# Optimization experiments

Measured on AMD Instinct MI355X. Metric: run time of the kernel, lower is better.

Reference implementation:

```python
import jax, jax.numpy as jnp
import numpy as np

OUT_DIM = 1024


def setup_inputs() -> dict:
    key = jax.random.key(0)
    k1, k2, k3, k4 = jax.random.split(key, 4)
    B, N, D = 4, 2048, 1024
    s = 1.0 / np.sqrt(D)
    return {
        "x": jax.random.normal(k1, (B, N, D), dtype=jnp.float32),
        "W_query": jax.random.normal(k2, (D, OUT_DIM), dtype=jnp.float32) * s,
        "W_key": jax.random.normal(k3, (D, OUT_DIM), dtype=jnp.float32) * s,
        "W_value": jax.random.normal(k4, (D, OUT_DIM), dtype=jnp.float32) * s,
    }


def reference(x, W_query, W_key, W_value):
    # x: [B, N, D_in]; W_*: [D_in, D_out] (torch Linear weight transposed)
    q = jnp.einsum("bnd,de->bne", x, W_query)
    k = jnp.einsum("bnd,de->bne", x, W_key)
    v = jnp.einsum("bnd,de->bne", x, W_value)
    sqrt_d = jnp.sqrt(jnp.asarray(OUT_DIM, dtype=jnp.float32))
    scores = jnp.einsum("bie,bje->bij", q, k) / sqrt_d  # [B, N, N]
    # NOTE: original uses softmax over dim=1 (query axis), not the usual dim=2
    attn = jax.nn.softmax(scores, axis=1)
    # dropout with train=False is identity (eval-mode reference)
    # out = attn^T @ v  ->  out[b, j] = sum_i attn[b, i, j] * v[b, i]
    return jnp.einsum("bij,bie->bje", attn, v)
```

## Files before the change

### kernel.cpp

```cpp
#include <hip/hip_runtime.h>
#include <math.h>


typedef __bf16 bf16x8 __attribute__((ext_vector_type(8)));
typedef float f32x4 __attribute__((ext_vector_type(4)));

static __device__ __forceinline__ unsigned short f2bf(float f) {
    unsigned u = __float_as_uint(f);
    u += 0x7fff + ((u >> 16) & 1);
    return (unsigned short)(u >> 16);
}

#define GLDS16(gptr, lptr)                                                            \
    __builtin_amdgcn_global_load_lds(                                                 \
        (const __attribute__((address_space(1))) void*)(gptr),                        \
        (__attribute__((address_space(3))) void*)(lptr), 16, 0, 0)

__device__ __forceinline__ void gemm256_core(
    const unsigned short* __restrict__ Ab,
    const unsigned short* __restrict__ Bb,
    const long ld, unsigned short* lds, f32x4 acc[8][4])
{
    const int tid  = threadIdx.x;
    const int w    = tid >> 6;
    const int lane = tid & 63;

    const int r  = lane >> 3;
    const int s  = lane & 7;
    const int cg = (s ^ r) * 8;

    const int fr    = lane & 15;
    const int quad  = lane >> 4;
    const int sw    = fr & 7;
    const int arow0 = (w >> 2) * 128;
    const int brow0 = (w & 3) * 64;

#define STG_A(t, mh, buf) do {                                              \
    const int rb_ = (w >> 2) * 128 + (mh) * 64 + (w & 3) * 16;              \
    const unsigned short* g_ = Ab + (long)(rb_ + r) * ld + (long)(t) * 64 + cg; \
    unsigned short* d_ = lds + (buf) * 16384 + rb_ * 64;                    \
    GLDS16(g_, d_); GLDS16(g_ + 8 * ld, d_ + 512); } while (0)
#define STG_B(t, nh, buf) do {                                              \
    const int rb_ = (w >> 1) * 64 + (nh) * 32 + (w & 1) * 16;               \
    const unsigned short* g_ = Bb + (long)(rb_ + r) * ld + (long)(t) * 64 + cg; \
    unsigned short* d_ = lds + 32768 + (buf) * 16384 + rb_ * 64;            \
    GLDS16(g_, d_); GLDS16(g_ + 8 * ld, d_ + 512); } while (0)

    bf16x8 af[4][2], bf[2][2];
#define LOADA(buf, mh) do {                                                 \
    _Pragma("unroll") for (int ks_ = 0; ks_ < 2; ks_++)                     \
    _Pragma("unroll") for (int i_ = 0; i_ < 4; i_++)                        \
        af[i_][ks_] = *(const bf16x8*)&lds[(buf) * 16384 +                  \
            (arow0 + (mh) * 64 + i_ * 16 + fr) * 64 +                       \
            ((ks_ * 4 + quad) ^ sw) * 8]; } while (0)
#define LOADB(buf, nh) do {                                                 \
    _Pragma("unroll") for (int ks_ = 0; ks_ < 2; ks_++)                     \
    _Pragma("unroll") for (int j_ = 0; j_ < 2; j_++)                        \
        bf[j_][ks_] = *(const bf16x8*)&lds[32768 + (buf) * 16384 +          \
            (brow0 + (nh) * 32 + j_ * 16 + fr) * 64 +                       \
            ((ks_ * 4 + quad) ^ sw) * 8]; } while (0)

#define MFMA16(mh, nh) do {                                                 \
    __builtin_amdgcn_s_setprio(1);                                          \
    _Pragma("unroll") for (int ks_ = 0; ks_ < 2; ks_++)                     \
    _Pragma("unroll") for (int i_ = 0; i_ < 4; i_++)                        \
    _Pragma("unroll") for (int j_ = 0; j_ < 2; j_++)                        \
        acc[(mh) * 4 + i_][(nh) * 2 + j_] =                                 \
            __builtin_amdgcn_mfma_f32_16x16x32_bf16(                        \
                af[i_][ks_], bf[j_][ks_],                                   \
                acc[(mh) * 4 + i_][(nh) * 2 + j_], 0, 0, 0);                \
    __builtin_amdgcn_s_setprio(0); } while (0)

#define BARSYNC  __builtin_amdgcn_s_barrier()
#define WAITLGKM do { asm volatile("s_waitcnt lgkmcnt(0)" ::: "memory");    \
                      __builtin_amdgcn_sched_barrier(0); } while (0)
#define WAITV4   asm volatile("s_waitcnt vmcnt(4)" ::: "memory")

#pragma unroll
    for (int i = 0; i < 8; i++)
#pragma unroll
        for (int j = 0; j < 4; j++) acc[i][j] = f32x4{0.f, 0.f, 0.f, 0.f};

    STG_A(0, 0, 0); STG_A(0, 1, 0); STG_B(0, 0, 0); STG_B(0, 1, 0);
    STG_A(1, 0, 1); STG_B(1, 1, 1);
    asm volatile("s_waitcnt vmcnt(4)" ::: "memory");
    BARSYNC;

#pragma unroll 1
    for (int i = 0; i < 8; ++i) {
        const int t1 = 2 * i + 1;
        const int t2 = (2 * i + 2) & 15;
        const int t3 = (2 * i + 3) & 15;
        LOADA(0, 0); LOADB(0, 0); STG_B(t1, 0, 1);
        BARSYNC; WAITLGKM; MFMA16(0, 0); BARSYNC;
        LOADB(0, 1); STG_A(t1, 1, 1);
        BARSYNC; WAITLGKM; MFMA16(0, 1); BARSYNC;
        LOADA(0, 1); STG_A(t2, 0, 0);
        BARSYNC; WAITLGKM; MFMA16(1, 1); BARSYNC;
        LOADB(0, 0); STG_B(t2, 1, 0);
        BARSYNC; WAITLGKM; MFMA16(1, 0); WAITV4; BARSYNC;
        LOADA(1, 0); LOADB(1, 0); STG_A(t2, 1, 0);
        BARSYNC; WAITLGKM; MFMA16(0, 0); BARSYNC;
        LOADB(1, 1); STG_B(t2, 0, 0);
        BARSYNC; WAITLGKM; MFMA16(0, 1); BARSYNC;
        LOADA(1, 1); STG_A(t3, 0, 1);
        BARSYNC; WAITLGKM; MFMA16(1, 1); BARSYNC;
        LOADB(1, 0); STG_B(t3, 1, 1);
        BARSYNC; WAITLGKM; MFMA16(1, 0); WAITV4; BARSYNC;
    }
    asm volatile("s_waitcnt vmcnt(0)" ::: "memory");

#undef STG_A
#undef STG_B
#undef LOADA
#undef LOADB
#undef MFMA16
#undef BARSYNC
#undef WAITLGKM
#undef WAITV4
}

__global__ __launch_bounds__(512, 2) void gemm_qkv256(
    const unsigned short* __restrict__ A, const unsigned short* __restrict__ B,
    unsigned short* __restrict__ QK, unsigned short* __restrict__ Vt)
{
    __shared__ unsigned short lds[65536];
    const int orig = blockIdx.x;
    const int xcd  = orig & 7;
    const int pos  = orig >> 3;
    const long gm0 = (long)(xcd * 4 + (pos & 3)) * 256;
    const long gn0 = (long)(pos >> 2) * 256;

    f32x4 acc[8][4];
    gemm256_core(A + gm0 * 1024, B + gn0 * 1024, 1024, lds, acc);

    const int tid = threadIdx.x;
    const int w = tid >> 6, lane = tid & 63;
    const int fr = lane & 15, quad = lane >> 4;
    const int wm = (w >> 2) * 128, wn = (w & 3) * 64;

    if (gn0 < 2048) {
#pragma unroll
        for (int mi = 0; mi < 8; mi++) {
            const long rb = gm0 + wm + (mi >> 2) * 64 + (mi & 3) * 16 + quad * 4;
#pragma unroll
            for (int n = 0; n < 4; n++) {
                const long cb = gn0 + wn + n * 16 + fr;
#pragma unroll
                for (int rr = 0; rr < 4; rr++)
                    QK[(rb + rr) * 2048L + cb] = f2bf(acc[mi][n][rr]);
            }
        }
    } else {
#pragma unroll
        for (int mi = 0; mi < 8; mi++) {
            const long rb = gm0 + wm + (mi >> 2) * 64 + (mi & 3) * 16 + quad * 4;
#pragma unroll
            for (int n = 0; n < 4; n++) {
                const long ce = gn0 - 2048 + wn + n * 16 + fr;
                ushort4 o;
                o.x = f2bf(acc[mi][n][0]);
                o.y = f2bf(acc[mi][n][1]);
                o.z = f2bf(acc[mi][n][2]);
                o.w = f2bf(acc[mi][n][3]);
                *(ushort4*)&Vt[ce * 8192L + rb] = o;
            }
        }
    }
}

__global__ __launch_bounds__(512, 2) void gemm_scores256(
    const unsigned short* __restrict__ QKb, unsigned short* __restrict__ P,
    float* __restrict__ l)
{
    __shared__ unsigned short lds[65536];
    const int orig = blockIdx.x;
    const int xcd  = orig & 7;
    const int pos  = orig >> 3;
    const int bz   = xcd >> 1;
    const long gm0 = (long)((xcd & 1) * 4 + (pos >> 3)) * 256;
    const long gn0 = (long)(pos & 7) * 256;

    const unsigned short* Ab = QKb + (long)bz * 2048 * 2048 + 1024 + gm0 * 2048;
    const unsigned short* Bb = QKb + (long)bz * 2048 * 2048 + gn0 * 2048;

    f32x4 acc[8][4];
    gemm256_core(Ab, Bb, 2048, lds, acc);

    const int tid = threadIdx.x;
    const int w = tid >> 6, lane = tid & 63;
    const int fr = lane & 15, quad = lane >> 4;
    const int wm = (w >> 2) * 128, wn = (w & 3) * 64;

    unsigned short* Pb = P + (long)bz * 2048 * 2048;
    float* lb = l + (long)bz * 2048;
    const float scale = 1.0f / 32.0f;
#pragma unroll
    for (int mi = 0; mi < 8; mi++) {
        const long rb = gm0 + wm + (mi >> 2) * 64 + (mi & 3) * 16 + quad * 4;
        float rs[4] = {0.f, 0.f, 0.f, 0.f};
#pragma unroll
        for (int n = 0; n < 4; n++) {
            const long cb = gn0 + wn + n * 16 + fr;
#pragma unroll
            for (int rr = 0; rr < 4; rr++) {
                float e = __expf(acc[mi][n][rr] * scale);
                rs[rr] += e;
                Pb[(rb + rr) * 2048L + cb] = f2bf(e);
            }
        }
#pragma unroll
        for (int rr = 0; rr < 4; rr++) {
#pragma unroll
            for (int m = 8; m > 0; m >>= 1) rs[rr] += __shfl_xor(rs[rr], m, 16);
        }
        if (fr == 0) {
#pragma unroll
            for (int rr = 0; rr < 4; rr++)
                atomicAdd(&lb[rb + rr], rs[rr]);
        }
    }
}

__global__ __launch_bounds__(256) void gemm_pv(
    const unsigned short* __restrict__ P, const unsigned short* __restrict__ Vt,
    const float* __restrict__ l, float* __restrict__ out)
{
    __shared__ unsigned short As[128 * 64];
    __shared__ unsigned short Bs[128 * 64];

    const int tid  = threadIdx.x;
    const int wave = tid >> 6;
    const int lane = tid & 63;
    const int bz   = blockIdx.z;
    const long gm0 = (long)blockIdx.y * 128;
    const long gn0 = (long)blockIdx.x * 128;

    const unsigned short* Ab = P + (long)bz * 2048 * 2048;
    const unsigned short* Bb = Vt + (long)bz * 2048;

    const int r = lane >> 3;
    const int s = lane & 7;
    const int cg = (s ^ r) * 8;
    const unsigned short* ap = Ab + (gm0 + wave * 32 + r) * 2048L + cg;
    const unsigned short* bp = Bb + (gn0 + wave * 32 + r) * 8192L + cg;
    unsigned short* asl = &As[wave * 2048];
    unsigned short* bsl = &Bs[wave * 2048];

    const int wm   = (wave & 1) * 64;
    const int wn   = (wave >> 1) * 64;
    const int fr   = lane & 15;
    const int quad = lane >> 4;
    const int sw   = fr & 7;

    f32x4 acc[4][4];
#pragma unroll
    for (int i = 0; i < 4; i++)
#pragma unroll
        for (int j = 0; j < 4; j++) acc[i][j] = f32x4{0.f, 0.f, 0.f, 0.f};

    for (int k0 = 0; k0 < 2048; k0 += 64) {
        GLDS16(ap, asl);
        GLDS16(ap + 8 * 2048L, asl + 512);
        GLDS16(ap + 16 * 2048L, asl + 1024);
        GLDS16(ap + 24 * 2048L, asl + 1536);
        GLDS16(bp, bsl);
        GLDS16(bp + 8 * 8192L, bsl + 512);
        GLDS16(bp + 16 * 8192L, bsl + 1024);
        GLDS16(bp + 24 * 8192L, bsl + 1536);
        ap += 64;
        bp += 64;
        __syncthreads();

#pragma unroll
        for (int t = 0; t < 2; t++) {
            const int qs = ((t * 4 + quad) ^ sw) * 8;
            bf16x8 af[4], bf[4];
#pragma unroll
            for (int i = 0; i < 4; i++)
                af[i] = *(const bf16x8*)&As[(wm + i * 16 + fr) * 64 + qs];
#pragma unroll
            for (int j = 0; j < 4; j++)
                bf[j] = *(const bf16x8*)&Bs[(wn + j * 16 + fr) * 64 + qs];
#pragma unroll
            for (int i = 0; i < 4; i++)
#pragma unroll
                for (int j = 0; j < 4; j++)
                    acc[i][j] = __builtin_amdgcn_mfma_f32_16x16x32_bf16(
                        af[i], bf[j], acc[i][j], 0, 0, 0);
        }
        __syncthreads();
    }

    float* Ob = out + (long)bz * 2048 * 1024;
    const float* lb = l + (long)bz * 2048;
    const long crow0 = gm0 + wm + quad * 4;
#pragma unroll
    for (int i = 0; i < 4; i++) {
        const long rb = crow0 + i * 16;
        float inv[4];
#pragma unroll
        for (int rr = 0; rr < 4; rr++) inv[rr] = 1.0f / lb[rb + rr];
#pragma unroll
        for (int j = 0; j < 4; j++) {
            const long cb = gn0 + wn + j * 16 + fr;
#pragma unroll
            for (int rr = 0; rr < 4; rr++)
                Ob[(rb + rr) * 1024L + cb] = acc[i][j][rr] * inv[rr];
        }
    }
}

__global__ __launch_bounds__(256) void prep(
    const float* __restrict__ x,
    const float* __restrict__ Wq, const float* __restrict__ Wk,
    const float* __restrict__ Wv,
    unsigned short* __restrict__ xb, unsigned short* __restrict__ Wqkvt,
    float* __restrict__ l)
{
    __shared__ float t[32][33];
    const int b = blockIdx.x;
    const int tid = threadIdx.x;
    if (b < 8192) {
        int i = b * 256 + tid;
        float4 v = ((const float4*)x)[i];
        ushort4 o;
        o.x = f2bf(v.x); o.y = f2bf(v.y); o.z = f2bf(v.z); o.w = f2bf(v.w);
        ((ushort4*)xb)[i] = o;
        return;
    }
    if (b == 8192 + 3072) {
        float4 z = {0.f, 0.f, 0.f, 0.f};
#pragma unroll
        for (int i = 0; i < 8; i++)
            ((float4*)l)[tid * 8 + i] = z;
        return;
    }
    int tix = b - 8192;
    const int w = tix >> 10;
    tix &= 1023;
    const float* W = (w == 0) ? Wq : (w == 1) ? Wk : Wv;
    unsigned short* Wt = Wqkvt + (long)w * 1024 * 1024;
    const int bx = (tix & 31) * 32;
    const int by = (tix >> 5) * 32;
    const int tx = tid & 31;
    const int ty = (tid >> 5) * 4;
#pragma unroll
    for (int j = 0; j < 4; j++)
        t[ty + j][tx] = W[(long)(by + ty + j) * 1024 + bx + tx];
    __syncthreads();
#pragma unroll
    for (int j = 0; j < 4; j++)
        Wt[(long)(bx + ty + j) * 1024 + by + tx] = f2bf(t[tx][ty + j]);
}

extern "C" void kernel_launch(void* const* d_in, const int* in_sizes, int n_in,
                              void* d_out, int out_size, void* d_ws,
                              size_t ws_size, hipStream_t stream)
{
    const float* x  = (const float*)d_in[0];
    const float* Wq = (const float*)d_in[1];
    const float* Wk = (const float*)d_in[2];
    const float* Wv = (const float*)d_in[3];
    float* out = (float*)d_out;

    const long M1 = 1024 * 1024;
    unsigned short* u     = (unsigned short*)d_ws;
    unsigned short* xb    = u;
    unsigned short* Wqkvt = u + 8 * M1;
    unsigned short* QKb   = Wqkvt + 3 * M1;
    unsigned short* Vtb   = QKb + 16 * M1;
    unsigned short* Pb    = Vtb + 8 * M1;
    float* l              = (float*)(Pb + 16 * M1);

    prep<<<dim3(8192 + 3072 + 1), dim3(256), 0, stream>>>(x, Wq, Wk, Wv, xb, Wqkvt, l);

    gemm_qkv256<<<dim3(384), dim3(512), 0, stream>>>(xb, Wqkvt, QKb, Vtb);

    gemm_scores256<<<dim3(256), dim3(512), 0, stream>>>(QKb, Pb, l);

    gemm_pv<<<dim3(8, 16, 4), dim3(256), 0, stream>>>(Pb, Vtb, l, out);
}
```

Measured before the change: 236.5 us.

## Widen QKV projection tile to 256x384 and double-buffer B fragments

```diff
diff --git a/kernel.cpp b/kernel.cpp
--- a/kernel.cpp
+++ b/kernel.cpp
@@ -15,6 +15,10 @@
     __builtin_amdgcn_global_load_lds(                                                 \
         (const __attribute__((address_space(1))) void*)(gptr),                        \
         (__attribute__((address_space(3))) void*)(lptr), 16, 0, 0)
+
+#define BARSYNC  __builtin_amdgcn_s_barrier()
+#define WAITLGKM do { asm volatile("s_waitcnt lgkmcnt(0)" ::: "memory");    \
+                      __builtin_amdgcn_sched_barrier(0); } while (0)
 
 __device__ __forceinline__ void gemm256_core(
     const unsigned short* __restrict__ Ab,
@@ -46,35 +50,30 @@
     unsigned short* d_ = lds + 32768 + (buf) * 16384 + rb_ * 64;            \
     GLDS16(g_, d_); GLDS16(g_ + 8 * ld, d_ + 512); } while (0)
 
-    bf16x8 af[4][2], bf[2][2];
+    bf16x8 af[4][2], bfA[2][2], bfB[2][2];
 #define LOADA(buf, mh) do {                                                 \
     _Pragma("unroll") for (int ks_ = 0; ks_ < 2; ks_++)                     \
     _Pragma("unroll") for (int i_ = 0; i_ < 4; i_++)                        \
         af[i_][ks_] = *(const bf16x8*)&lds[(buf) * 16384 +                  \
             (arow0 + (mh) * 64 + i_ * 16 + fr) * 64 +                       \
             ((ks_ * 4 + quad) ^ sw) * 8]; } while (0)
-#define LOADB(buf, nh) do {                                                 \
+#define LOADB(BF, buf, nh) do {                                             \
     _Pragma("unroll") for (int ks_ = 0; ks_ < 2; ks_++)                     \
     _Pragma("unroll") for (int j_ = 0; j_ < 2; j_++)                        \
-        bf[j_][ks_] = *(const bf16x8*)&lds[32768 + (buf) * 16384 +          \
+        BF[j_][ks_] = *(const bf16x8*)&lds[32768 + (buf) * 16384 +          \
             (brow0 + (nh) * 32 + j_ * 16 + fr) * 64 +                       \
             ((ks_ * 4 + quad) ^ sw) * 8]; } while (0)
 
-#define MFMA16(mh, nh) do {                                                 \
+#define MFMA16(mh, nh, BF) do {                                             \
     __builtin_amdgcn_s_setprio(1);                                          \
     _Pragma("unroll") for (int ks_ = 0; ks_ < 2; ks_++)                     \
     _Pragma("unroll") for (int i_ = 0; i_ < 4; i_++)                        \
     _Pragma("unroll") for (int j_ = 0; j_ < 2; j_++)                        \
         acc[(mh) * 4 + i_][(nh) * 2 + j_] =                                 \
             __builtin_amdgcn_mfma_f32_16x16x32_bf16(                        \
-                af[i_][ks_], bf[j_][ks_],                                   \
+                af[i_][ks_], BF[j_][ks_],                                   \
                 acc[(mh) * 4 + i_][(nh) * 2 + j_], 0, 0, 0);                \
     __builtin_amdgcn_s_setprio(0); } while (0)
-
-#define BARSYNC  __builtin_amdgcn_s_barrier()
-#define WAITLGKM do { asm volatile("s_waitcnt lgkmcnt(0)" ::: "memory");    \
-                      __builtin_amdgcn_sched_barrier(0); } while (0)
-#define WAITV4   asm volatile("s_waitcnt vmcnt(4)" ::: "memory")
 
 #pragma unroll
     for (int i = 0; i < 8; i++)
@@ -91,22 +90,24 @@
         const int t1 = 2 * i + 1;
         const int t2 = (2 * i + 2) & 15;
         const int t3 = (2 * i + 3) & 15;
-        LOADA(0, 0); LOADB(0, 0); STG_B(t1, 0, 1);
-        BARSYNC; WAITLGKM; MFMA16(0, 0); BARSYNC;
-        LOADB(0, 1); STG_A(t1, 1, 1);
-        BARSYNC; WAITLGKM; MFMA16(0, 1); BARSYNC;
+        LOADA(0, 0); LOADB(bfA, 0, 0); STG_B(t1, 0, 1);
+        BARSYNC; WAITLGKM; MFMA16(0, 0, bfA); BARSYNC;
+        LOADB(bfB, 0, 1); STG_A(t1, 1, 1);
+        BARSYNC; WAITLGKM; MFMA16(0, 1, bfB); BARSYNC;
         LOADA(0, 1); STG_A(t2, 0, 0);
-        BARSYNC; WAITLGKM; MFMA16(1, 1); BARSYNC;
-        LOADB(0, 0); STG_B(t2, 1, 0);
-        BARSYNC; WAITLGKM; MFMA16(1, 0); WAITV4; BARSYNC;
-        LOADA(1, 0); LOADB(1, 0); STG_A(t2, 1, 0);
-        BARSYNC; WAITLGKM; MFMA16(0, 0); BARSYNC;
-        LOADB(1, 1); STG_B(t2, 0, 0);
-        BARSYNC; WAITLGKM; MFMA16(0, 1); BARSYNC;
+        BARSYNC; WAITLGKM; MFMA16(1, 1, bfB); BARSYNC;
+        STG_B(t2, 1, 0);
+        BARSYNC; MFMA16(1, 0, bfA);
+        asm volatile("s_waitcnt vmcnt(4)" ::: "memory"); BARSYNC;
+        LOADA(1, 0); LOADB(bfA, 1, 0); STG_A(t2, 1, 0);
+        BARSYNC; WAITLGKM; MFMA16(0, 0, bfA); BARSYNC;
+        LOADB(bfB, 1, 1); STG_B(t2, 0, 0);
+        BARSYNC; WAITLGKM; MFMA16(0, 1, bfB); BARSYNC;
         LOADA(1, 1); STG_A(t3, 0, 1);
-        BARSYNC; WAITLGKM; MFMA16(1, 1); BARSYNC;
-        LOADB(1, 0); STG_B(t3, 1, 1);
-        BARSYNC; WAITLGKM; MFMA16(1, 0); WAITV4; BARSYNC;
+        BARSYNC; WAITLGKM; MFMA16(1, 1, bfB); BARSYNC;
+        STG_B(t3, 1, 1);
+        BARSYNC; MFMA16(1, 0, bfA);
+        asm volatile("s_waitcnt vmcnt(4)" ::: "memory"); BARSYNC;
     }
     asm volatile("s_waitcnt vmcnt(0)" ::: "memory");
 
@@ -115,54 +116,144 @@
 #undef LOADA
 #undef LOADB
 #undef MFMA16
-#undef BARSYNC
-#undef WAITLGKM
-#undef WAITV4
-}
-
-__global__ __launch_bounds__(512, 2) void gemm_qkv256(
+}
+
+__device__ __forceinline__ void gemm384_core(
+    const unsigned short* __restrict__ Ab,
+    const unsigned short* __restrict__ Bb,
+    const long ld, unsigned short* lds, f32x4 acc[8][6])
+{
+    const int tid  = threadIdx.x;
+    const int w    = tid >> 6;
+    const int lane = tid & 63;
+
+    const int r  = lane >> 3;
+    const int s  = lane & 7;
+    const int cg = (s ^ r) * 8;
+
+    const int fr    = lane & 15;
+    const int quad  = lane >> 4;
+    const int sw    = fr & 7;
+    const int arow0 = (w >> 2) * 128;
+    const int brow0 = (w & 3) * 96;
+
+#define STG_A3(t, mh, buf) do {                                             \
+    const int rb_ = (w >> 2) * 128 + (mh) * 64 + (w & 3) * 16;              \
+    const unsigned short* g_ = Ab + (long)(rb_ + r) * ld + (long)(t) * 64 + cg; \
+    unsigned short* d_ = lds + (buf) * 16384 + rb_ * 64;                    \
+    GLDS16(g_, d_); GLDS16(g_ + 8 * ld, d_ + 512); } while (0)
+#define STG_B3(t, nh, buf) do {                                             \
+    _Pragma("unroll") for (int q_ = 0; q_ < 3; q_++) {                      \
+        const int u_ = w * 3 + q_;                                          \
+        const int row0_ = (u_ & 3) * 96 + (nh) * 48 + (u_ >> 2) * 8;        \
+        const unsigned short* g_ = Bb + (long)(row0_ + r) * ld + (long)(t) * 64 + cg; \
+        unsigned short* d_ = lds + 32768 + (buf) * 24576 + row0_ * 64;      \
+        GLDS16(g_, d_); } } while (0)
+
+    bf16x8 af[4][2], bfA[3][2], bfB[3][2];
+#define LOADA3(buf, mh) do {                                                \
+    _Pragma("unroll") for (int ks_ = 0; ks_ < 2; ks_++)                     \
+    _Pragma("unroll") for (int i_ = 0; i_ < 4; i_++)                        \
+        af[i_][ks_] = *(const bf16x8*)&lds[(buf) * 16384 +                  \
+            (arow0 + (mh) * 64 + i_ * 16 + fr) * 64 +                       \
+            ((ks_ * 4 + quad) ^ sw) * 8]; } while (0)
+#define LOADB3(BF, buf, nh) do {                                            \
+    _Pragma("unroll") for (int ks_ = 0; ks_ < 2; ks_++)                     \
+    _Pragma("unroll") for (int j_ = 0; j_ < 3; j_++)                        \
+        BF[j_][ks_] = *(const bf16x8*)&lds[32768 + (buf) * 24576 +          \
+            (brow0 + (nh) * 48 + j_ * 16 + fr) * 64 +                       \
+            ((ks_ * 4 + quad) ^ sw) * 8]; } while (0)
+
+#define MFMA24(mh, nh, BF) do {                                             \
+    __builtin_amdgcn_s_setprio(1);                                          \
+    _Pragma("unroll") for (int ks_ = 0; ks_ < 2; ks_++)                     \
+    _Pragma("unroll") for (int i_ = 0; i_ < 4; i_++)                        \
+    _Pragma("unroll") for (int j_ = 0; j_ < 3; j_++)                        \
+        acc[(mh) * 4 + i_][(nh) * 3 + j_] =                                 \
+            __builtin_amdgcn_mfma_f32_16x16x32_bf16(                        \
+                af[i_][ks_], BF[j_][ks_],                                   \
+                acc[(mh) * 4 + i_][(nh) * 3 + j_], 0, 0, 0);                \
+    __builtin_amdgcn_s_setprio(0); } while (0)
+
+#pragma unroll
+    for (int i = 0; i < 8; i++)
+#pragma unroll
+        for (int j = 0; j < 6; j++) acc[i][j] = f32x4{0.f, 0.f, 0.f, 0.f};
+
+    STG_A3(0, 0, 0); STG_A3(0, 1, 0); STG_B3(0, 0, 0); STG_B3(0, 1, 0);
+    STG_A3(1, 0, 1); STG_B3(1, 1, 1);
+    asm volatile("s_waitcnt vmcnt(5)" ::: "memory");
+    BARSYNC;
+
+#pragma unroll 1
+    for (int i = 0; i < 8; ++i) {
+        const int t1 = 2 * i + 1;
+        const int t2 = (2 * i + 2) & 15;
+        const int t3 = (2 * i + 3) & 15;
+        LOADA3(0, 0); LOADB3(bfA, 0, 0); STG_B3(t1, 0, 1);
+        BARSYNC; WAITLGKM; MFMA24(0, 0, bfA); BARSYNC;
+        LOADB3(bfB, 0, 1); STG_A3(t1, 1, 1);
+        BARSYNC; WAITLGKM; MFMA24(0, 1, bfB); BARSYNC;
+        LOADA3(0, 1); STG_A3(t2, 0, 0);
+        BARSYNC; WAITLGKM; MFMA24(1, 1, bfB); BARSYNC;
+        STG_B3(t2, 1, 0);
+        BARSYNC; MFMA24(1, 0, bfA);
+        asm volatile("s_waitcnt vmcnt(5)" ::: "memory"); BARSYNC;
+        LOADA3(1, 0); LOADB3(bfA, 1, 0); STG_A3(t2, 1, 0);
+        BARSYNC; WAITLGKM; MFMA24(0, 0, bfA); BARSYNC;
+        LOADB3(bfB, 1, 1); STG_B3(t2, 0, 0);
+        BARSYNC; WAITLGKM; MFMA24(0, 1, bfB); BARSYNC;
+        LOADA3(1, 1); STG_A3(t3, 0, 1);
+        BARSYNC; WAITLGKM; MFMA24(1, 1, bfB); BARSYNC;
+        STG_B3(t3, 1, 1);
+        BARSYNC; MFMA24(1, 0, bfA);
+        asm volatile("s_waitcnt vmcnt(5)" ::: "memory"); BARSYNC;
+    }
+    asm volatile("s_waitcnt vmcnt(0)" ::: "memory");
+
+#undef STG_A3
+#undef STG_B3
+#undef LOADA3
+#undef LOADB3
+#undef MFMA24
+}
+
+__global__ __launch_bounds__(512, 2) void gemm_qkv384(
     const unsigned short* __restrict__ A, const unsigned short* __restrict__ B,
     unsigned short* __restrict__ QK, unsigned short* __restrict__ Vt)
 {
-    __shared__ unsigned short lds[65536];
+    __shared__ unsigned short lds[81920];
     const int orig = blockIdx.x;
     const int xcd  = orig & 7;
     const int pos  = orig >> 3;
     const long gm0 = (long)(xcd * 4 + (pos & 3)) * 256;
-    const long gn0 = (long)(pos >> 2) * 256;
-
-    f32x4 acc[8][4];
-    gemm256_core(A + gm0 * 1024, B + gn0 * 1024, 1024, lds, acc);
+    const long gn0 = (long)(pos >> 2) * 384;
+
+    f32x4 acc[8][6];
+    gemm384_core(A + gm0 * 1024, B + gn0 * 1024, 1024, lds, acc);
 
     const int tid = threadIdx.x;
     const int w = tid >> 6, lane = tid & 63;
     const int fr = lane & 15, quad = lane >> 4;
-    const int wm = (w >> 2) * 128, wn = (w & 3) * 64;
-
-    if (gn0 < 2048) {
-#pragma unroll
-        for (int mi = 0; mi < 8; mi++) {
-            const long rb = gm0 + wm + (mi >> 2) * 64 + (mi & 3) * 16 + quad * 4;
-#pragma unroll
-            for (int n = 0; n < 4; n++) {
-                const long cb = gn0 + wn + n * 16 + fr;
+    const int wm = (w >> 2) * 128, wn = (w & 3) * 96;
+
+#pragma unroll
+    for (int mi = 0; mi < 8; mi++) {
+        const long rb = gm0 + wm + (mi >> 2) * 64 + (mi & 3) * 16 + quad * 4;
+#pragma unroll
+        for (int nj = 0; nj < 6; nj++) {
+            const long cb = gn0 + wn + nj * 16 + fr;
+            if (cb < 2048) {
 #pragma unroll
                 for (int rr = 0; rr < 4; rr++)
-                    QK[(rb + rr) * 2048L + cb] = f2bf(acc[mi][n][rr]);
-            }
-        }
-    } else {
-#pragma unroll
-        for (int mi = 0; mi < 8; mi++) {
-            const long rb = gm0 + wm + (mi >> 2) * 64 + (mi & 3) * 16 + quad * 4;
-#pragma unroll
-            for (int n = 0; n < 4; n++) {
-                const long ce = gn0 - 2048 + wn + n * 16 + fr;
+                    QK[(rb + rr) * 2048L + cb] = f2bf(acc[mi][nj][rr]);
+            } else {
+                const long ce = cb - 2048;
                 ushort4 o;
-                o.x = f2bf(acc[mi][n][0]);
-                o.y = f2bf(acc[mi][n][1]);
-                o.z = f2bf(acc[mi][n][2]);
-                o.w = f2bf(acc[mi][n][3]);
+                o.x = f2bf(acc[mi][nj][0]);
+                o.y = f2bf(acc[mi][nj][1]);
+                o.z = f2bf(acc[mi][nj][2]);
+                o.w = f2bf(acc[mi][nj][3]);
                 *(ushort4*)&Vt[ce * 8192L + rb] = o;
             }
         }
@@ -375,7 +466,7 @@
 
     prep<<<dim3(8192 + 3072 + 1), dim3(256), 0, stream>>>(x, Wq, Wk, Wv, xb, Wqkvt, l);
 
-    gemm_qkv256<<<dim3(384), dim3(512), 0, stream>>>(xb, Wqkvt, QKb, Vtb);
+    gemm_qkv384<<<dim3(256), dim3(512), 0, stream>>>(xb, Wqkvt, QKb, Vtb);
 
     gemm_scores256<<<dim3(256), dim3(512), 0, stream>>>(QKb, Pb, l);
 
```

Result: slower. 389.2 us (+64.6%).

## Port PV GEMM to pipelined 256x128 tile core and reuse B fragments in QKV loop

Applied to the files above, without the earlier changes.

```diff
diff --git a/kernel.cpp b/kernel.cpp
--- a/kernel.cpp
+++ b/kernel.cpp
@@ -15,6 +15,10 @@
     __builtin_amdgcn_global_load_lds(                                                 \
         (const __attribute__((address_space(1))) void*)(gptr),                        \
         (__attribute__((address_space(3))) void*)(lptr), 16, 0, 0)
+
+#define BARSYNC  __builtin_amdgcn_s_barrier()
+#define WAITLGKM do { asm volatile("s_waitcnt lgkmcnt(0)" ::: "memory");    \
+                      __builtin_amdgcn_sched_barrier(0); } while (0)
 
 __device__ __forceinline__ void gemm256_core(
     const unsigned short* __restrict__ Ab,
@@ -46,35 +50,30 @@
     unsigned short* d_ = lds + 32768 + (buf) * 16384 + rb_ * 64;            \
     GLDS16(g_, d_); GLDS16(g_ + 8 * ld, d_ + 512); } while (0)
 
-    bf16x8 af[4][2], bf[2][2];
+    bf16x8 af[4][2], bfA[2][2], bfB[2][2];
 #define LOADA(buf, mh) do {                                                 \
     _Pragma("unroll") for (int ks_ = 0; ks_ < 2; ks_++)                     \
     _Pragma("unroll") for (int i_ = 0; i_ < 4; i_++)                        \
         af[i_][ks_] = *(const bf16x8*)&lds[(buf) * 16384 +                  \
             (arow0 + (mh) * 64 + i_ * 16 + fr) * 64 +                       \
             ((ks_ * 4 + quad) ^ sw) * 8]; } while (0)
-#define LOADB(buf, nh) do {                                                 \
+#define LOADB(BF, buf, nh) do {                                             \
     _Pragma("unroll") for (int ks_ = 0; ks_ < 2; ks_++)                     \
     _Pragma("unroll") for (int j_ = 0; j_ < 2; j_++)                        \
-        bf[j_][ks_] = *(const bf16x8*)&lds[32768 + (buf) * 16384 +          \
+        BF[j_][ks_] = *(const bf16x8*)&lds[32768 + (buf) * 16384 +          \
             (brow0 + (nh) * 32 + j_ * 16 + fr) * 64 +                       \
             ((ks_ * 4 + quad) ^ sw) * 8]; } while (0)
 
-#define MFMA16(mh, nh) do {                                                 \
+#define MFMA16(mh, nh, BF) do {                                             \
     __builtin_amdgcn_s_setprio(1);                                          \
     _Pragma("unroll") for (int ks_ = 0; ks_ < 2; ks_++)                     \
     _Pragma("unroll") for (int i_ = 0; i_ < 4; i_++)                        \
     _Pragma("unroll") for (int j_ = 0; j_ < 2; j_++)                        \
         acc[(mh) * 4 + i_][(nh) * 2 + j_] =                                 \
             __builtin_amdgcn_mfma_f32_16x16x32_bf16(                        \
-                af[i_][ks_], bf[j_][ks_],                                   \
+                af[i_][ks_], BF[j_][ks_],                                   \
                 acc[(mh) * 4 + i_][(nh) * 2 + j_], 0, 0, 0);                \
     __builtin_amdgcn_s_setprio(0); } while (0)
-
-#define BARSYNC  __builtin_amdgcn_s_barrier()
-#define WAITLGKM do { asm volatile("s_waitcnt lgkmcnt(0)" ::: "memory");    \
-                      __builtin_amdgcn_sched_barrier(0); } while (0)
-#define WAITV4   asm volatile("s_waitcnt vmcnt(4)" ::: "memory")
 
 #pragma unroll
     for (int i = 0; i < 8; i++)
@@ -91,22 +90,24 @@
         const int t1 = 2 * i + 1;
         const int t2 = (2 * i + 2) & 15;
         const int t3 = (2 * i + 3) & 15;
-        LOADA(0, 0); LOADB(0, 0); STG_B(t1, 0, 1);
-        BARSYNC; WAITLGKM; MFMA16(0, 0); BARSYNC;
-        LOADB(0, 1); STG_A(t1, 1, 1);
-        BARSYNC; WAITLGKM; MFMA16(0, 1); BARSYNC;
+        LOADA(0, 0); LOADB(bfA, 0, 0); STG_B(t1, 0, 1);
+        BARSYNC; WAITLGKM; MFMA16(0, 0, bfA); BARSYNC;
+        LOADB(bfB, 0, 1); STG_A(t1, 1, 1);
+        BARSYNC; WAITLGKM; MFMA16(0, 1, bfB); BARSYNC;
         LOADA(0, 1); STG_A(t2, 0, 0);
-        BARSYNC; WAITLGKM; MFMA16(1, 1); BARSYNC;
-        LOADB(0, 0); STG_B(t2, 1, 0);
-        BARSYNC; WAITLGKM; MFMA16(1, 0); WAITV4; BARSYNC;
-        LOADA(1, 0); LOADB(1, 0); STG_A(t2, 1, 0);
-        BARSYNC; WAITLGKM; MFMA16(0, 0); BARSYNC;
-        LOADB(1, 1); STG_B(t2, 0, 0);
-        BARSYNC; WAITLGKM; MFMA16(0, 1); BARSYNC;
+        BARSYNC; WAITLGKM; MFMA16(1, 1, bfB); BARSYNC;
+        STG_B(t2, 1, 0);
+        BARSYNC; MFMA16(1, 0, bfA);
+        asm volatile("s_waitcnt vmcnt(4)" ::: "memory"); BARSYNC;
+        LOADA(1, 0); LOADB(bfA, 1, 0); STG_A(t2, 1, 0);
+        BARSYNC; WAITLGKM; MFMA16(0, 0, bfA); BARSYNC;
+        LOADB(bfB, 1, 1); STG_B(t2, 0, 0);
+        BARSYNC; WAITLGKM; MFMA16(0, 1, bfB); BARSYNC;
         LOADA(1, 1); STG_A(t3, 0, 1);
-        BARSYNC; WAITLGKM; MFMA16(1, 1); BARSYNC;
-        LOADB(1, 0); STG_B(t3, 1, 1);
-        BARSYNC; WAITLGKM; MFMA16(1, 0); WAITV4; BARSYNC;
+        BARSYNC; WAITLGKM; MFMA16(1, 1, bfB); BARSYNC;
+        STG_B(t3, 1, 1);
+        BARSYNC; MFMA16(1, 0, bfA);
+        asm volatile("s_waitcnt vmcnt(4)" ::: "memory"); BARSYNC;
     }
     asm volatile("s_waitcnt vmcnt(0)" ::: "memory");
 
@@ -115,9 +116,100 @@
 #undef LOADA
 #undef LOADB
 #undef MFMA16
-#undef BARSYNC
-#undef WAITLGKM
-#undef WAITV4
+}
+
+__device__ __forceinline__ void pv256_core(
+    const unsigned short* __restrict__ Ab,
+    const unsigned short* __restrict__ Bb,
+    unsigned short* lds, f32x4 acc[8][2])
+{
+    const int tid  = threadIdx.x;
+    const int w    = tid >> 6;
+    const int lane = tid & 63;
+
+    const int r  = lane >> 3;
+    const int s  = lane & 7;
+    const int cg = (s ^ r) * 8;
+
+    const int fr    = lane & 15;
+    const int quad  = lane >> 4;
+    const int sw    = fr & 7;
+    const int arow0 = (w >> 2) * 128;
+    const int brow0 = (w & 3) * 32;
+
+#define STG_PA(t, mh, buf) do {                                             \
+    const int rb_ = (w >> 2) * 128 + (mh) * 64 + (w & 3) * 16;              \
+    const unsigned short* g_ = Ab + (long)(rb_ + r) * 2048 + (long)(t) * 64 + cg; \
+    unsigned short* d_ = lds + (buf) * 16384 + rb_ * 64;                    \
+    GLDS16(g_, d_); GLDS16(g_ + 8 * 2048, d_ + 512); } while (0)
+#define STG_PB(t, nh, buf) do {                                             \
+    const int rb_ = (w & 3) * 32 + (nh) * 16 + (w >> 2) * 8;                \
+    const unsigned short* g_ = Bb + (long)(rb_ + r) * 8192 + (long)(t) * 64 + cg; \
+    unsigned short* d_ = lds + 32768 + (buf) * 8192 + rb_ * 64;             \
+    GLDS16(g_, d_); } while (0)
+
+    bf16x8 af[4][2], bfA[2], bfB[2];
+#define LOADPA(buf, mh) do {                                                \
+    _Pragma("unroll") for (int ks_ = 0; ks_ < 2; ks_++)                     \
+    _Pragma("unroll") for (int i_ = 0; i_ < 4; i_++)                        \
+        af[i_][ks_] = *(const bf16x8*)&lds[(buf) * 16384 +                  \
+            (arow0 + (mh) * 64 + i_ * 16 + fr) * 64 +                       \
+            ((ks_ * 4 + quad) ^ sw) * 8]; } while (0)
+#define LOADPB(BF, buf, nh) do {                                            \
+    _Pragma("unroll") for (int ks_ = 0; ks_ < 2; ks_++)                     \
+        BF[ks_] = *(const bf16x8*)&lds[32768 + (buf) * 8192 +               \
+            (brow0 + (nh) * 16 + fr) * 64 +                                 \
+            ((ks_ * 4 + quad) ^ sw) * 8]; } while (0)
+
+#define MFMA8(mh, nh, BF) do {                                              \
+    __builtin_amdgcn_s_setprio(1);                                          \
+    _Pragma("unroll") for (int ks_ = 0; ks_ < 2; ks_++)                     \
+    _Pragma("unroll") for (int i_ = 0; i_ < 4; i_++)                        \
+        acc[(mh) * 4 + i_][nh] = __builtin_amdgcn_mfma_f32_16x16x32_bf16(   \
+            af[i_][ks_], BF[ks_], acc[(mh) * 4 + i_][nh], 0, 0, 0);         \
+    __builtin_amdgcn_s_setprio(0); } while (0)
+
+#pragma unroll
+    for (int i = 0; i < 8; i++)
+#pragma unroll
+        for (int j = 0; j < 2; j++) acc[i][j] = f32x4{0.f, 0.f, 0.f, 0.f};
+
+    STG_PA(0, 0, 0); STG_PA(0, 1, 0); STG_PB(0, 0, 0); STG_PB(0, 1, 0);
+    STG_PA(1, 0, 1); STG_PB(1, 1, 1);
+    asm volatile("s_waitcnt vmcnt(3)" ::: "memory");
+    BARSYNC;
+
+#pragma unroll 1
+    for (int i = 0; i < 16; ++i) {
+        const int t1 = 2 * i + 1;
+        const int t2 = (2 * i + 2) & 31;
+        const int t3 = (2 * i + 3) & 31;
+        LOADPA(0, 0); LOADPB(bfA, 0, 0); STG_PB(t1, 0, 1);
+        BARSYNC; WAITLGKM; MFMA8(0, 0, bfA); BARSYNC;
+        LOADPB(bfB, 0, 1); STG_PA(t1, 1, 1);
+        BARSYNC; WAITLGKM; MFMA8(0, 1, bfB); BARSYNC;
+        LOADPA(0, 1); STG_PA(t2, 0, 0);
+        BARSYNC; WAITLGKM; MFMA8(1, 1, bfB); BARSYNC;
+        STG_PB(t2, 1, 0);
+        BARSYNC; MFMA8(1, 0, bfA);
+        asm volatile("s_waitcnt vmcnt(3)" ::: "memory"); BARSYNC;
+        LOADPA(1, 0); LOADPB(bfA, 1, 0); STG_PA(t2, 1, 0);
+        BARSYNC; WAITLGKM; MFMA8(0, 0, bfA); BARSYNC;
+        LOADPB(bfB, 1, 1); STG_PB(t2, 0, 0);
+        BARSYNC; WAITLGKM; MFMA8(0, 1, bfB); BARSYNC;
+        LOADPA(1, 1); STG_PA(t3, 0, 1);
+        BARSYNC; WAITLGKM; MFMA8(1, 1, bfB); BARSYNC;
+        STG_PB(t3, 1, 1);
+        BARSYNC; MFMA8(1, 0, bfA);
+        asm volatile("s_waitcnt vmcnt(3)" ::: "memory"); BARSYNC;
+    }
+    asm volatile("s_waitcnt vmcnt(0)" ::: "memory");
+
+#undef STG_PA
+#undef STG_PB
+#undef LOADPA
+#undef LOADPB
+#undef MFMA8
 }
 
 __global__ __launch_bounds__(512, 2) void gemm_qkv256(
@@ -222,91 +314,43 @@
     }
 }
 
-__global__ __launch_bounds__(256) void gemm_pv(
+__global__ __launch_bounds__(512, 2) void gemm_pv256(
     const unsigned short* __restrict__ P, const unsigned short* __restrict__ Vt,
     const float* __restrict__ l, float* __restrict__ out)
 {
-    __shared__ unsigned short As[128 * 64];
-    __shared__ unsigned short Bs[128 * 64];
-
-    const int tid  = threadIdx.x;
-    const int wave = tid >> 6;
-    const int lane = tid & 63;
-    const int bz   = blockIdx.z;
-    const long gm0 = (long)blockIdx.y * 128;
-    const long gn0 = (long)blockIdx.x * 128;
-
-    const unsigned short* Ab = P + (long)bz * 2048 * 2048;
-    const unsigned short* Bb = Vt + (long)bz * 2048;
-
-    const int r = lane >> 3;
-    const int s = lane & 7;
-    const int cg = (s ^ r) * 8;
-    const unsigned short* ap = Ab + (gm0 + wave * 32 + r) * 2048L + cg;
-    const unsigned short* bp = Bb + (gn0 + wave * 32 + r) * 8192L + cg;
-    unsigned short* asl = &As[wave * 2048];
-    unsigned short* bsl = &Bs[wave * 2048];
-
-    const int wm   = (wave & 1) * 64;
-    const int wn   = (wave >> 1) * 64;
-    const int fr   = lane & 15;
-    const int quad = lane >> 4;
-    const int sw   = fr & 7;
-
-    f32x4 acc[4][4];
-#pragma unroll
-    for (int i = 0; i < 4; i++)
-#pragma unroll
-        for (int j = 0; j < 4; j++) acc[i][j] = f32x4{0.f, 0.f, 0.f, 0.f};
-
-    for (int k0 = 0; k0 < 2048; k0 += 64) {
-        GLDS16(ap, asl);
-        GLDS16(ap + 8 * 2048L, asl + 512);
-        GLDS16(ap + 16 * 2048L, asl + 1024);
-        GLDS16(ap + 24 * 2048L, asl + 1536);
-        GLDS16(bp, bsl);
-        GLDS16(bp + 8 * 8192L, bsl + 512);
-        GLDS16(bp + 16 * 8192L, bsl + 1024);
-        GLDS16(bp + 24 * 8192L, bsl + 1536);
-        ap += 64;
-        bp += 64;
-        __syncthreads();
-
-#pragma unroll
-        for (int t = 0; t < 2; t++) {
-            const int qs = ((t * 4 + quad) ^ sw) * 8;
-            bf16x8 af[4], bf[4];
-#pragma unroll
-            for (int i = 0; i < 4; i++)
-                af[i] = *(const bf16x8*)&As[(wm + i * 16 + fr) * 64 + qs];
-#pragma unroll
-            for (int j = 0; j < 4; j++)
-                bf[j] = *(const bf16x8*)&Bs[(wn + j * 16 + fr) * 64 + qs];
-#pragma unroll
-            for (int i = 0; i < 4; i++)
-#pragma unroll
-                for (int j = 0; j < 4; j++)
-                    acc[i][j] = __builtin_amdgcn_mfma_f32_16x16x32_bf16(
-                        af[i], bf[j], acc[i][j], 0, 0, 0);
-        }
-        __syncthreads();
-    }
+    __shared__ unsigned short lds[49152];
+    const int orig = blockIdx.x;
+    const int xcd  = orig & 7;
+    const int pos  = orig >> 3;
+    const int bz   = xcd >> 1;
+    const long gm0 = (long)((xcd & 1) * 4 + (pos >> 3)) * 256;
+    const long gn0 = (long)(pos & 7) * 128;
+
+    const unsigned short* Ab = P + (long)bz * 2048 * 2048 + gm0 * 2048;
+    const unsigned short* Bb = Vt + gn0 * 8192 + (long)bz * 2048;
+
+    f32x4 acc[8][2];
+    pv256_core(Ab, Bb, lds, acc);
+
+    const int tid = threadIdx.x;
+    const int w = tid >> 6, lane = tid & 63;
+    const int fr = lane & 15, quad = lane >> 4;
+    const int wm = (w >> 2) * 128, wn = (w & 3) * 32;
 
     float* Ob = out + (long)bz * 2048 * 1024;
     const float* lb = l + (long)bz * 2048;
-    const long crow0 = gm0 + wm + quad * 4;
-#pragma unroll
-    for (int i = 0; i < 4; i++) {
-        const long rb = crow0 + i * 16;
+#pragma unroll
+    for (int mi = 0; mi < 8; mi++) {
+        const long rb = gm0 + wm + (mi >> 2) * 64 + (mi & 3) * 16 + quad * 4;
         float inv[4];
 #pragma unroll
         for (int rr = 0; rr < 4; rr++) inv[rr] = 1.0f / lb[rb + rr];
 #pragma unroll
-        for (int j = 0; j < 4; j++) {
-            const long cb = gn0 + wn + j * 16 + fr;
+        for (int nj = 0; nj < 2; nj++) {
+            const long cb = gn0 + wn + nj * 16 + fr;
 #pragma unroll
             for (int rr = 0; rr < 4; rr++)
-                Ob[(rb + rr) * 1024L + cb] = acc[i][j][rr] * inv[rr];
+                Ob[(rb + rr) * 1024L + cb] = acc[mi][nj][rr] * inv[rr];
         }
     }
 }
@@ -379,5 +423,5 @@
 
     gemm_scores256<<<dim3(256), dim3(512), 0, stream>>>(QKb, Pb, l);
 
-    gemm_pv<<<dim3(8, 16, 4), dim3(256), 0, stream>>>(Pb, Vtb, l, out);
-}
+    gemm_pv256<<<dim3(256), dim3(512), 0, stream>>>(Pb, Vtb, l, out);
+}
```

New measurement: 227.4 us. 1.04x faster.
